# Kernel optimization log

Measured on AMD Instinct MI355X. Metric: run time of the kernel, lower is better.

The kernel has to match this reference:

```python
import jax, jax.numpy as jnp
import numpy as np

CLAMP_MIN, CLAMP_MAX = -3.0, 3.0
RANK = 16


def setup_inputs() -> dict:
    key = jax.random.key(0)
    ks = jax.random.split(key, 8)
    B, N, D, H, R = 8, 4096, 1024, 256, RANK
    s = 0.02  # small weight std so clamp/exp are well-conditioned
    return {
        "query_emb": jax.random.normal(ks[0], (B, D), jnp.float32),
        "context_embs": jax.random.normal(ks[1], (B, N, D), jnp.float32),
        "W1": jax.random.normal(ks[2], (D, H), jnp.float32) * s,
        "b1": jnp.zeros((H,), jnp.float32),
        "Wd": jax.random.normal(ks[3], (H, D), jnp.float32) * s,
        "bd": jnp.zeros((D,), jnp.float32),
        "WL": jax.random.normal(ks[4], (H, D * R), jnp.float32) * s,
        "bL": jnp.zeros((D * R,), jnp.float32),
        "Wdel": jax.random.normal(ks[5], (H, D), jnp.float32) * s,
        "bdel": jnp.zeros((D,), jnp.float32),
        "Wa": jax.random.normal(ks[6], (H, D), jnp.float32) * s,
        "ba": jnp.zeros((D,), jnp.float32),
    }


def reference(query_emb, context_embs, W1, b1, Wd, bd, WL, bL, Wdel, bdel, Wa, ba):
    B, N, D = context_embs.shape
    R = RANK
    # Backbone: Linear + ReLU (assumed MLP backbone)
    h = jax.nn.relu(query_emb @ W1 + b1)                      # (B,H)
    # Parameter heads (SkewGaussian.forward)
    log_d = jnp.clip(h @ Wd + bd, CLAMP_MIN, CLAMP_MAX)       # (B,D)
    L = (h @ WL + bL).reshape(B, D, R) * 0.1                  # (B,D,R)
    delta = (h @ Wdel + bdel) * 0.1                           # (B,D)
    alpha = h @ Wa + ba                                       # (B,D)

    mu = query_emb + delta                                    # (B,D)
    diff = context_embs - mu[:, None, :]                      # (B,N,D)
    d_inv = jnp.exp(-log_d)                                   # (B,D)

    # Diagonal Mahalanobis term
    mahal_diag = jnp.einsum('bnd,bd->bn', diff * diff, d_inv) # (B,N)

    # Woodbury correction with small RxR system per batch
    DinvL = d_inv[:, :, None] * L                             # (B,D,R)
    M = jnp.eye(R, dtype=L.dtype)[None] + jnp.einsum('bdr,bds->brs', L, DinvL)  # (B,R,R)
    M_inv = jnp.linalg.inv(M)
    v = diff * d_inv[:, None, :]                              # (B,N,D)
    w = jnp.einsum('bdr,bnd->brn', L, v)                      # (B,R,N)
    correction = jnp.sum(w * jnp.einsum('brs,bsn->brn', M_inv, w), axis=1)  # (B,N)

    mahal = mahal_diag - correction
    log_det = jnp.sum(log_d, axis=-1, keepdims=True) + jnp.linalg.slogdet(M)[1][:, None]  # (B,1)
    symmetric_score = -0.5 * (mahal + log_det)                # (B,N)

    skew_input = jnp.einsum('bd,bnd->bn', alpha, diff)
    skew_score = jax.nn.log_sigmoid(skew_input)
    return symmetric_score + skew_score
```

## Files before the change

### kernel.cpp

```cpp
#include <hip/hip_runtime.h>
#include <math.h>

#define BB 8
#define NN 4096
#define DD 1024
#define HH 256
#define RR 16

#define WS_GT      0
#define WS_MU      131072
#define WS_DINV    139264
#define WS_ALPHA   147456
#define WS_HP      155648
#define WS_LDP     188416
#define WS_MINV    188544
#define WS_LOGDET  190592
#define WS_L       190608

__global__ __launch_bounds__(256) void ka1_h(
    const float* __restrict__ qe, const float* __restrict__ W1, float* __restrict__ ws)
{
    const int b = blockIdx.x >> 4;
    const int sl = blockIdx.x & 15;
    const int c = threadIdx.x;
    __shared__ float qe_s[64];
    if (c < 64) qe_s[c] = qe[b * DD + sl * 64 + c];
    __syncthreads();
    float a0 = 0.f, a1 = 0.f, a2 = 0.f, a3 = 0.f;
    const float* W1p = W1 + (sl * 64) * HH;
    #pragma unroll 4
    for (int dl = 0; dl < 64; dl += 4) {
        a0 = fmaf(qe_s[dl + 0], W1p[(dl + 0) * HH + c], a0);
        a1 = fmaf(qe_s[dl + 1], W1p[(dl + 1) * HH + c], a1);
        a2 = fmaf(qe_s[dl + 2], W1p[(dl + 2) * HH + c], a2);
        a3 = fmaf(qe_s[dl + 3], W1p[(dl + 3) * HH + c], a3);
    }
    ws[WS_HP + (b * 16 + sl) * HH + c] = (a0 + a1) + (a2 + a3);
}

__global__ __launch_bounds__(256) void ka2_heads(
    const float* __restrict__ qe, const float* __restrict__ b1,
    const float* __restrict__ Wd, const float* __restrict__ bd,
    const float* __restrict__ WL, const float* __restrict__ bL,
    const float* __restrict__ Wdel, const float* __restrict__ bdel,
    const float* __restrict__ Wa, const float* __restrict__ ba,
    float* __restrict__ ws)
{
    __shared__ float h_s[BB * HH];
    __shared__ float red[4][512];
    const int tid = threadIdx.x;

    for (int i = tid; i < BB * HH; i += 256) {
        const int bb = i >> 8, c = i & 255;
        float v = b1[c];
        #pragma unroll
        for (int k = 0; k < 16; ++k) v += ws[WS_HP + (bb * 16 + k) * HH + c];
        h_s[i] = fmaxf(v, 0.f);
    }
    __syncthreads();

    const int blk = blockIdx.x;
    const int lane = tid & 63;
    const int u = tid >> 6;

    int mode; const float* W; const float* bias; int base;
    if (blk < 16)       { mode = 0; W = Wd;   bias = bd;   base = 0;  }
    else if (blk < 32)  { mode = 1; W = Wdel; bias = bdel; base = 16; }
    else if (blk < 48)  { mode = 2; W = Wa;   bias = ba;   base = 32; }
    else                { mode = 3; W = WL;   bias = bL;   base = 48; }
    const int ld = (mode == 3) ? (DD * RR) : DD;
    const int cc = (blk - base) * 64 + lane;

    float acc[8];
    #pragma unroll
    for (int b = 0; b < 8; ++b) acc[b] = 0.f;

    #pragma unroll 4
    for (int rr = 0; rr < 64; ++rr) {
        const int r = u * 64 + rr;
        const float wv = W[r * ld + cc];
        #pragma unroll
        for (int b = 0; b < 8; ++b) acc[b] = fmaf(h_s[b * HH + r], wv, acc[b]);
    }
    #pragma unroll
    for (int b = 0; b < 8; ++b) red[u][lane * 8 + b] = acc[b];
    __syncthreads();

    for (int e = tid; e < 512; e += 256) {
        const int cl = e >> 3, bb = e & 7;
        const int cm = (blk - base) * 64 + cl;
        float s = red[0][e] + red[1][e] + red[2][e] + red[3][e] + bias[cm];
        if (mode == 0) {
            const float ldv = fminf(fmaxf(s, -3.f), 3.f);
            ws[WS_DINV + bb * DD + cm] = expf(-ldv);
            red[0][e] = ldv;
        } else if (mode == 1) {
            ws[WS_MU + bb * DD + cm] = qe[bb * DD + cm] + 0.1f * s;
        } else if (mode == 2) {
            ws[WS_ALPHA + bb * DD + cm] = s;
        } else {
            ws[WS_L + bb * (DD * RR) + cm] = 0.1f * s;
        }
    }
    if (mode == 0) {
        __syncthreads();
        if (tid < 8) {
            float s = 0.f;
            for (int cl = 0; cl < 64; ++cl) s += red[0][cl * 8 + tid];
            ws[WS_LDP + blk * 8 + tid] = s;
        }
    }
}

__global__ __launch_bounds__(256) void kg_gt(float* __restrict__ ws)
{
    const int idx = blockIdx.x * 256 + threadIdx.x;
    const int d = idx & (DD - 1);
    const int r = (idx >> 10) & (RR - 1);
    const int b = idx >> 14;
    ws[WS_GT + idx] = ws[WS_DINV + b * DD + d] * ws[WS_L + (b * DD + d) * RR + r];
}

__global__ __launch_bounds__(1024) void kMGJ(float* __restrict__ ws)
{
    const int b = blockIdx.x;
    const int tid = threadIdx.x;
    const int dgr = tid >> 8;
    const int gs = tid & 255;
    const int g = gs >> 4, s = gs & 15;

    const float* Gt = ws + WS_GT + (size_t)b * (RR * DD);
    const float* Lp = ws + WS_L + (size_t)b * (DD * RR);

    float acc = 0.f;
    #pragma unroll 8
    for (int k = 0; k < 256; ++k) {
        const int d = dgr * 256 + k;
        acc = fmaf(Gt[g * DD + d], Lp[d * 16 + s], acc);
    }

    __shared__ float Mp[4][256];
    __shared__ float A[16][33];
    Mp[dgr][gs] = acc;
    __syncthreads();

    const bool act = (tid < 256);
    if (act) {
        A[g][s] = ((g == s) ? 1.f : 0.f) + Mp[0][gs] + Mp[1][gs] + Mp[2][gs] + Mp[3][gs];
        A[g][s + 16] = (g == s) ? 1.f : 0.f;
    }
    __syncthreads();

    float logdetM = 0.f;
    for (int k = 0; k < 16; ++k) {
        const float piv = A[k][k];
        if (tid == 0) logdetM += logf(piv);
        __syncthreads();
        if (act && g == k) {
            const float rinv = 1.f / piv;
            A[g][s] *= rinv;
            A[g][s + 16] *= rinv;
        }
        __syncthreads();
        const float f = (act && g != k) ? A[g][k] : 0.f;
        __syncthreads();
        if (act && g != k) {
            A[g][s]      = fmaf(-f, A[k][s],      A[g][s]);
            A[g][s + 16] = fmaf(-f, A[k][s + 16], A[g][s + 16]);
        }
        __syncthreads();
    }
    if (act) ws[WS_MINV + b * 256 + g * 16 + s] = A[g][s + 16];
    if (tid == 0) {
        float lds = 0.f;
        for (int k = 0; k < 16; ++k) lds += ws[WS_LDP + k * 8 + b];
        ws[WS_LOGDET + b] = lds + logdetM;
    }
}

__global__ __launch_bounds__(512, 2) void kc_main(
    const float* __restrict__ ctx, const float* __restrict__ ws, float* __restrict__ out)
{
    const int bid = blockIdx.x;
    const int b = bid >> 7;
    const int tile = bid & 127;
    const int wave = threadIdx.x >> 6;
    const int lane = threadIdx.x & 63;
    const int n0 = tile * 32 + wave * 4;

    __shared__ float gt_s[RR * DD];
    {
        float4* gs4 = (float4*)gt_s;
        const float4* Gt4g = (const float4*)(ws + WS_GT + (size_t)b * (RR * DD));
        for (int i = threadIdx.x; i < RR * DD / 4; i += 512) gs4[i] = Gt4g[i];
    }
    __syncthreads();
    const float4* gs4 = (const float4*)gt_s;

    const float4* mu4 = (const float4*)(ws + WS_MU + b * DD);
    const float4* dv4 = (const float4*)(ws + WS_DINV + b * DD);
    const float4* al4 = (const float4*)(ws + WS_ALPHA + b * DD);
    const float4* ctx4 = (const float4*)(ctx + ((size_t)(b * NN + n0)) * DD);

    float g[4][16];
    float md[4], aa[4];
    #pragma unroll
    for (int i = 0; i < 4; ++i) {
        md[i] = 0.f; aa[i] = 0.f;
        #pragma unroll
        for (int r = 0; r < 16; ++r) g[i][r] = 0.f;
    }

    #pragma unroll 2
    for (int step = 0; step < 4; ++step) {
        const int fi = step * 64 + lane;
        const float4 c0 = ctx4[0 * (DD / 4) + fi];
        const float4 c1 = ctx4[1 * (DD / 4) + fi];
        const float4 c2 = ctx4[2 * (DD / 4) + fi];
        const float4 c3 = ctx4[3 * (DD / 4) + fi];
        const float4 mv = mu4[fi];

        float diff[4][4];
        diff[0][0] = c0.x - mv.x; diff[0][1] = c0.y - mv.y; diff[0][2] = c0.z - mv.z; diff[0][3] = c0.w - mv.w;
        diff[1][0] = c1.x - mv.x; diff[1][1] = c1.y - mv.y; diff[1][2] = c1.z - mv.z; diff[1][3] = c1.w - mv.w;
        diff[2][0] = c2.x - mv.x; diff[2][1] = c2.y - mv.y; diff[2][2] = c2.z - mv.z; diff[2][3] = c2.w - mv.w;
        diff[3][0] = c3.x - mv.x; diff[3][1] = c3.y - mv.y; diff[3][2] = c3.z - mv.z; diff[3][3] = c3.w - mv.w;

        {
            const float4 dvv = dv4[fi];
            const float4 av = al4[fi];
            const float dva[4] = {dvv.x, dvv.y, dvv.z, dvv.w};
            const float ava[4] = {av.x, av.y, av.z, av.w};
            #pragma unroll
            for (int i = 0; i < 4; ++i) {
                #pragma unroll
                for (int j = 0; j < 4; ++j) {
                    md[i] = fmaf(diff[i][j] * dva[j], diff[i][j], md[i]);
                    aa[i] = fmaf(ava[j], diff[i][j], aa[i]);
                }
            }
        }

        #pragma unroll
        for (int r = 0; r < 16; ++r) {
            const float4 gt = gs4[r * 256 + fi];
            #pragma unroll
            for (int i = 0; i < 4; ++i) {
                g[i][r] = fmaf(gt.x, diff[i][0], g[i][r]);
                g[i][r] = fmaf(gt.y, diff[i][1], g[i][r]);
                g[i][r] = fmaf(gt.z, diff[i][2], g[i][r]);
                g[i][r] = fmaf(gt.w, diff[i][3], g[i][r]);
            }
        }
    }

    float v[64];
    #pragma unroll
    for (int i = 0; i < 4; ++i)
        #pragma unroll
        for (int r = 0; r < 16; ++r) v[i * 16 + r] = g[i][r];

    #pragma unroll
    for (int s6 = 0; s6 < 6; ++s6) {
        const int m = 1 << s6;
        const int half = 32 >> s6;
        const bool up = (lane & m) != 0;
        #pragma unroll
        for (int ii = 0; ii < half; ++ii) {
            float x0 = v[2 * ii], x1 = v[2 * ii + 1];
            float y0 = __shfl_xor(x0, m, 64);
            float y1 = __shfl_xor(x1, m, 64);
            v[ii] = up ? (x1 + y1) : (x0 + y0);
        }
    }
    const float w = v[0];

    #pragma unroll
    for (int m = 1; m < 64; m <<= 1) {
        #pragma unroll
        for (int i = 0; i < 4; ++i) {
            md[i] += __shfl_xor(md[i], m, 64);
            aa[i] += __shfl_xor(aa[i], m, 64);
        }
    }

    const int r = lane & 15;
    const int rowbase = lane & 48;
    const float* Minv = ws + WS_MINV + b * 256 + r * 16;
    float y = 0.f;
    #pragma unroll
    for (int s = 0; s < 16; ++s) y = fmaf(Minv[s], __shfl(w, rowbase + s, 64), y);
    float corr = w * y;
    corr += __shfl_xor(corr, 1, 64);
    corr += __shfl_xor(corr, 2, 64);
    corr += __shfl_xor(corr, 4, 64);
    corr += __shfl_xor(corr, 8, 64);

    const float ld = ws[WS_LOGDET + b];
    if ((lane & 15) == 0) {
        const int i = lane >> 4;
        const float mdv = (i & 2) ? ((i & 1) ? md[3] : md[2]) : ((i & 1) ? md[1] : md[0]);
        const float aav = (i & 2) ? ((i & 1) ? aa[3] : aa[2]) : ((i & 1) ? aa[1] : aa[0]);
        const float lsig = fminf(aav, 0.f) - log1pf(expf(-fabsf(aav)));
        out[(size_t)b * NN + n0 + i] = -0.5f * (mdv - corr + ld) + lsig;
    }
}

extern "C" void kernel_launch(void* const* d_in, const int* in_sizes, int n_in,
                              void* d_out, int out_size, void* d_ws, size_t ws_size,
                              hipStream_t stream)
{
    const float* qe   = (const float*)d_in[0];
    const float* ctx  = (const float*)d_in[1];
    const float* W1   = (const float*)d_in[2];
    const float* b1   = (const float*)d_in[3];
    const float* Wd   = (const float*)d_in[4];
    const float* bd   = (const float*)d_in[5];
    const float* WL   = (const float*)d_in[6];
    const float* bL   = (const float*)d_in[7];
    const float* Wdel = (const float*)d_in[8];
    const float* bdel = (const float*)d_in[9];
    const float* Wa   = (const float*)d_in[10];
    const float* ba   = (const float*)d_in[11];
    float* out = (float*)d_out;
    float* ws  = (float*)d_ws;

    ka1_h<<<128, 256, 0, stream>>>(qe, W1, ws);
    ka2_heads<<<304, 256, 0, stream>>>(qe, b1, Wd, bd, WL, bL, Wdel, bdel, Wa, ba, ws);
    kg_gt<<<512, 256, 0, stream>>>(ws);
    kMGJ<<<8, 1024, 0, stream>>>(ws);
    kc_main<<<1024, 512, 0, stream>>>(ctx, ws, out);
}
```

Before: 285.8 us.

## Stage context tiles into LDS via async global_load_lds double buffering

After: 282.6 us. Within noise of the previous version (-1.1%).

```diff
diff --git a/kernel.cpp b/kernel.cpp
--- a/kernel.cpp
+++ b/kernel.cpp
@@ -16,6 +16,9 @@
 #define WS_MINV    188544
 #define WS_LOGDET  190592
 #define WS_L       190608
+
+typedef __attribute__((address_space(3))) unsigned int lds_uint;
+typedef __attribute__((address_space(1))) const unsigned int g_uint;
 
 __global__ __launch_bounds__(256) void ka1_h(
     const float* __restrict__ qe, const float* __restrict__ W1, float* __restrict__ ws)
@@ -184,86 +187,93 @@
     const int bid = blockIdx.x;
     const int b = bid >> 7;
     const int tile = bid & 127;
-    const int wave = threadIdx.x >> 6;
-    const int lane = threadIdx.x & 63;
-    const int n0 = tile * 32 + wave * 4;
+    const int tid = threadIdx.x;
+    const int wave = tid >> 6;
+    const int lane = tid & 63;
+    const int n0 = tile * 32;
 
     __shared__ float gt_s[RR * DD];
+    __shared__ float cbuf[2][32 * 64];
+
     {
-        float4* gs4 = (float4*)gt_s;
-        const float4* Gt4g = (const float4*)(ws + WS_GT + (size_t)b * (RR * DD));
-        for (int i = threadIdx.x; i < RR * DD / 4; i += 512) gs4[i] = Gt4g[i];
-    }
-    __syncthreads();
-    const float4* gs4 = (const float4*)gt_s;
-
+        const float* gtg = ws + WS_GT + (size_t)b * (RR * DD);
+        #pragma unroll
+        for (int k = 0; k < 8; ++k) {
+            __builtin_amdgcn_global_load_lds(
+                (g_uint*)(gtg + (size_t)(k * 512 + wave * 64 + lane) * 4),
+                (lds_uint*)((unsigned int*)gt_s + (k * 512 + wave * 64) * 4),
+                16, 0, 0);
+        }
+        const int row = tid >> 4, f4 = tid & 15;
+        const float* src = ctx + ((size_t)(b * NN + n0 + row)) * DD + (0 * 64) + ((f4 ^ (row & 7)) * 4);
+        __builtin_amdgcn_global_load_lds(
+            (g_uint*)src,
+            (lds_uint*)((unsigned int*)&cbuf[0][0] + (wave * 64) * 4),
+            16, 0, 0);
+    }
+    asm volatile("s_waitcnt vmcnt(0)" ::: "memory");
+    __syncthreads();
+
+    const int rl = lane >> 4;
+    const int row_blk = wave * 4 + rl;
+    const int f4 = lane & 15;
+    const float4* gt4 = (const float4*)gt_s;
     const float4* mu4 = (const float4*)(ws + WS_MU + b * DD);
     const float4* dv4 = (const float4*)(ws + WS_DINV + b * DD);
     const float4* al4 = (const float4*)(ws + WS_ALPHA + b * DD);
-    const float4* ctx4 = (const float4*)(ctx + ((size_t)(b * NN + n0)) * DD);
-
-    float g[4][16];
-    float md[4], aa[4];
-    #pragma unroll
-    for (int i = 0; i < 4; ++i) {
-        md[i] = 0.f; aa[i] = 0.f;
-        #pragma unroll
-        for (int r = 0; r < 16; ++r) g[i][r] = 0.f;
-    }
-
-    #pragma unroll 2
-    for (int step = 0; step < 4; ++step) {
-        const int fi = step * 64 + lane;
-        const float4 c0 = ctx4[0 * (DD / 4) + fi];
-        const float4 c1 = ctx4[1 * (DD / 4) + fi];
-        const float4 c2 = ctx4[2 * (DD / 4) + fi];
-        const float4 c3 = ctx4[3 * (DD / 4) + fi];
+
+    float g[16];
+    #pragma unroll
+    for (int r = 0; r < 16; ++r) g[r] = 0.f;
+    float md = 0.f, aa = 0.f;
+
+    const int stage_row = tid >> 4, stage_f4 = tid & 15;
+    const float* stage_base = ctx + ((size_t)(b * NN + n0 + stage_row)) * DD + ((stage_f4 ^ (stage_row & 7)) * 4);
+
+    for (int t = 0; t < 16; ++t) {
+        if (t + 1 < 16) {
+            __builtin_amdgcn_global_load_lds(
+                (g_uint*)(stage_base + (t + 1) * 64),
+                (lds_uint*)((unsigned int*)&cbuf[(t + 1) & 1][0] + (wave * 64) * 4),
+                16, 0, 0);
+            asm volatile("s_waitcnt vmcnt(1)" ::: "memory");
+        } else {
+            asm volatile("s_waitcnt vmcnt(0)" ::: "memory");
+        }
+        __syncthreads();
+
+        const int fi = t * 16 + f4;
+        const float4* cb4 = (const float4*)&cbuf[t & 1][0];
+        const float4 cv = cb4[row_blk * 16 + (f4 ^ (row_blk & 7))];
         const float4 mv = mu4[fi];
-
-        float diff[4][4];
-        diff[0][0] = c0.x - mv.x; diff[0][1] = c0.y - mv.y; diff[0][2] = c0.z - mv.z; diff[0][3] = c0.w - mv.w;
-        diff[1][0] = c1.x - mv.x; diff[1][1] = c1.y - mv.y; diff[1][2] = c1.z - mv.z; diff[1][3] = c1.w - mv.w;
-        diff[2][0] = c2.x - mv.x; diff[2][1] = c2.y - mv.y; diff[2][2] = c2.z - mv.z; diff[2][3] = c2.w - mv.w;
-        diff[3][0] = c3.x - mv.x; diff[3][1] = c3.y - mv.y; diff[3][2] = c3.z - mv.z; diff[3][3] = c3.w - mv.w;
-
-        {
-            const float4 dvv = dv4[fi];
-            const float4 av = al4[fi];
-            const float dva[4] = {dvv.x, dvv.y, dvv.z, dvv.w};
-            const float ava[4] = {av.x, av.y, av.z, av.w};
-            #pragma unroll
-            for (int i = 0; i < 4; ++i) {
-                #pragma unroll
-                for (int j = 0; j < 4; ++j) {
-                    md[i] = fmaf(diff[i][j] * dva[j], diff[i][j], md[i]);
-                    aa[i] = fmaf(ava[j], diff[i][j], aa[i]);
-                }
-            }
-        }
+        const float4 dvv = dv4[fi];
+        const float4 av = al4[fi];
+
+        const float d0 = cv.x - mv.x, d1 = cv.y - mv.y, d2 = cv.z - mv.z, d3 = cv.w - mv.w;
+        md = fmaf(d0 * dvv.x, d0, md); md = fmaf(d1 * dvv.y, d1, md);
+        md = fmaf(d2 * dvv.z, d2, md); md = fmaf(d3 * dvv.w, d3, md);
+        aa = fmaf(av.x, d0, aa); aa = fmaf(av.y, d1, aa);
+        aa = fmaf(av.z, d2, aa); aa = fmaf(av.w, d3, aa);
 
         #pragma unroll
         for (int r = 0; r < 16; ++r) {
-            const float4 gt = gs4[r * 256 + fi];
-            #pragma unroll
-            for (int i = 0; i < 4; ++i) {
-                g[i][r] = fmaf(gt.x, diff[i][0], g[i][r]);
-                g[i][r] = fmaf(gt.y, diff[i][1], g[i][r]);
-                g[i][r] = fmaf(gt.z, diff[i][2], g[i][r]);
-                g[i][r] = fmaf(gt.w, diff[i][3], g[i][r]);
-            }
-        }
-    }
-
-    float v[64];
-    #pragma unroll
-    for (int i = 0; i < 4; ++i)
-        #pragma unroll
-        for (int r = 0; r < 16; ++r) v[i * 16 + r] = g[i][r];
-
-    #pragma unroll
-    for (int s6 = 0; s6 < 6; ++s6) {
-        const int m = 1 << s6;
-        const int half = 32 >> s6;
+            const float4 gt = gt4[r * 256 + fi];
+            g[r] = fmaf(gt.x, d0, g[r]);
+            g[r] = fmaf(gt.y, d1, g[r]);
+            g[r] = fmaf(gt.z, d2, g[r]);
+            g[r] = fmaf(gt.w, d3, g[r]);
+        }
+        __syncthreads();
+    }
+
+    float v[16];
+    #pragma unroll
+    for (int r = 0; r < 16; ++r) v[r] = g[r];
+
+    #pragma unroll
+    for (int s4 = 0; s4 < 4; ++s4) {
+        const int m = 1 << s4;
+        const int half = 8 >> s4;
         const bool up = (lane & m) != 0;
         #pragma unroll
         for (int ii = 0; ii < half; ++ii) {
@@ -276,33 +286,27 @@
     const float w = v[0];
 
     #pragma unroll
-    for (int m = 1; m < 64; m <<= 1) {
-        #pragma unroll
-        for (int i = 0; i < 4; ++i) {
-            md[i] += __shfl_xor(md[i], m, 64);
-            aa[i] += __shfl_xor(aa[i], m, 64);
-        }
+    for (int m = 1; m < 16; m <<= 1) {
+        md += __shfl_xor(md, m, 64);
+        aa += __shfl_xor(aa, m, 64);
     }
 
     const int r = lane & 15;
-    const int rowbase = lane & 48;
+    const int base16 = lane & 48;
     const float* Minv = ws + WS_MINV + b * 256 + r * 16;
     float y = 0.f;
     #pragma unroll
-    for (int s = 0; s < 16; ++s) y = fmaf(Minv[s], __shfl(w, rowbase + s, 64), y);
+    for (int s = 0; s < 16; ++s) y = fmaf(Minv[s], __shfl(w, base16 + s, 64), y);
     float corr = w * y;
     corr += __shfl_xor(corr, 1, 64);
     corr += __shfl_xor(corr, 2, 64);
     corr += __shfl_xor(corr, 4, 64);
     corr += __shfl_xor(corr, 8, 64);
 
-    const float ld = ws[WS_LOGDET + b];
-    if ((lane & 15) == 0) {
-        const int i = lane >> 4;
-        const float mdv = (i & 2) ? ((i & 1) ? md[3] : md[2]) : ((i & 1) ? md[1] : md[0]);
-        const float aav = (i & 2) ? ((i & 1) ? aa[3] : aa[2]) : ((i & 1) ? aa[1] : aa[0]);
-        const float lsig = fminf(aav, 0.f) - log1pf(expf(-fabsf(aav)));
-        out[(size_t)b * NN + n0 + i] = -0.5f * (mdv - corr + ld) + lsig;
+    if (f4 == 0) {
+        const float ld = ws[WS_LOGDET + b];
+        const float lsig = fminf(aa, 0.f) - log1pf(expf(-fabsf(aa)));
+        out[(size_t)b * NN + n0 + row_blk] = -0.5f * (md - corr + ld) + lsig;
     }
 }
 
```
